# Kernel tuning notes

Hardware: AMD Instinct MI355X
Metric: run time of the kernel (lower is better)

## Reference

```python
import jax, jax.numpy as jnp
import numpy as np
from jax import lax

B, C, H, W = 8, 64, 128, 128
KS = 3          # kernel size
K = KS * KS     # kernel field = 9
PAD = 1


def conv2d(x, w, b):
    # x: [B,Cin,H,W], w: [Cout,Cin,kh,kw], 'same' 3x3 conv
    y = lax.conv_general_dilated(x, w, window_strides=(1, 1),
                                 padding=((PAD, PAD), (PAD, PAD)),
                                 dimension_numbers=('NCHW', 'OIHW', 'NCHW'))
    return y + b[None, :, None, None]


def modulated_deform_conv(x, offset, mask, weight, bias):
    # x:[B,C,H,W], offset:[B,2K,H,W] (dy,dx per tap), mask:[B,K,H,W]
    Bs, Cin, Hin, Win = x.shape
    off = offset.reshape(Bs, K, 2, Hin, Win)
    ky, kx = jnp.meshgrid(jnp.arange(KS), jnp.arange(KS), indexing='ij')
    ky = ky.reshape(K).astype(x.dtype)   # kernel tap row offsets 0..2
    kx = kx.reshape(K).astype(x.dtype)
    # sampling positions p = p0 + p_k + offset (stride=1, pad=1)
    py = (jnp.arange(Hin, dtype=x.dtype)[None, None, :, None] - PAD
          + ky[None, :, None, None] + off[:, :, 0])            # [B,K,H,W]
    px = (jnp.arange(Win, dtype=x.dtype)[None, None, None, :] - PAD
          + kx[None, :, None, None] + off[:, :, 1])            # [B,K,H,W]

    y0 = jnp.floor(py); x0 = jnp.floor(px)
    ly = py - y0; lx = px - x0                                  # frac parts
    y0i = y0.astype(jnp.int32); x0i = x0.astype(jnp.int32)

    x_flat = x.reshape(Bs, Cin, Hin * Win)

    def gather(iy, ix):
        valid = ((iy >= 0) & (iy < Hin) & (ix >= 0) & (ix < Win))
        flat = (jnp.clip(iy, 0, Hin - 1) * Win + jnp.clip(ix, 0, Win - 1))
        g = jax.vmap(lambda xb, ib: xb[:, ib])(x_flat, flat.reshape(Bs, -1))
        g = g.reshape(Bs, Cin, K, Hin, Win)
        return g * valid[:, None].astype(x.dtype)

    w00 = ((1 - ly) * (1 - lx))[:, None]  # [B,1,K,H,W]
    w01 = ((1 - ly) * lx)[:, None]
    w10 = (ly * (1 - lx))[:, None]
    w11 = (ly * lx)[:, None]

    val = (w00 * gather(y0i, x0i) + w01 * gather(y0i, x0i + 1)
           + w10 * gather(y0i + 1, x0i) + w11 * gather(y0i + 1, x0i + 1))
    val = val * mask[:, None]                                   # modulation
    out = jnp.einsum('ock,bckhw->bohw', weight.reshape(weight.shape[0], Cin, K), val)
    return out + bias[None, :, None, None]


def setup_inputs() -> dict:
    key = jax.random.key(0)
    ks = jax.random.split(key, 7)
    s = 0.05
    return {
        'x': jax.random.normal(ks[0], (B, C, H, W), jnp.float32),
        'w_om': jax.random.normal(ks[1], (3 * K, C, KS, KS), jnp.float32) * s,
        'b_om': jax.random.normal(ks[2], (3 * K,), jnp.float32) * s,
        'w_dc': jax.random.normal(ks[3], (C, C, KS, KS), jnp.float32) * s,
        'b_dc': jax.random.normal(ks[4], (C,), jnp.float32) * s,
        'w_c': jax.random.normal(ks[5], (C, C, KS, KS), jnp.float32) * s,
        'b_c': jax.random.normal(ks[6], (C,), jnp.float32) * s,
    }


def reference(x, w_om, b_om, w_dc, b_dc, w_c, b_c):
    om = conv2d(x, w_om, b_om)                       # [B,3K,H,W]
    offset, mask_raw = om[:, :2 * K], om[:, 2 * K:]
    mask = 2.0 * jax.nn.sigmoid(mask_raw)
    out = modulated_deform_conv(x, offset, mask, w_dc, b_dc)
    act = jnp.where(out > 0, out, 0.2 * out)         # LeakyReLU(0.2)
    return conv2d(act, w_c, b_c) + x
```

## Files before the change

### kernel.cpp

```cpp
#include <hip/hip_runtime.h>
#include <math.h>

#define Bn 8
#define Cn 64
#define Hn 128
#define Wn 128
#define HWn (Hn * Wn)

#define WOM_OFF 0
#define WDC_OFF 18432
#define WC_OFF 55296

typedef __attribute__((ext_vector_type(8))) short short8;
typedef __attribute__((ext_vector_type(4))) float floatx4;

__device__ __forceinline__ float bf2f(short s) {
  return __uint_as_float(((unsigned)(unsigned short)s) << 16);
}
__device__ __forceinline__ short f2bf(float f) {
  unsigned u = __float_as_uint(f);
  u += 0x7fff + ((u >> 16) & 1);
  return (short)(u >> 16);
}

__global__ __launch_bounds__(256) void k_prep_w(
    const float* __restrict__ w_om, const float* __restrict__ w_dc,
    const float* __restrict__ w_c, short* __restrict__ wt) {
  int idx = blockIdx.x * 256 + threadIdx.x;
  if (idx >= 92160) return;
  float v;
  if (idx < WDC_OFF) {
    int e = idx;
    int elem = e & 7, lane = (e >> 3) & 63, mt = (e >> 9) & 1, t = e >> 10;
    int kk = t % 9, cc = t / 9;
    int row = mt * 16 + (lane & 15);
    int cin = cc * 32 + (lane >> 4) * 8 + elem;
    v = (row < 27) ? w_om[(row * 64 + cin) * 9 + kk] : 0.f;
  } else {
    int e = (idx < WC_OFF) ? idx - WDC_OFF : idx - WC_OFF;
    const float* src = (idx < WC_OFF) ? w_dc : w_c;
    int elem = e & 7, lane = (e >> 3) & 63, mt = (e >> 9) & 3, t = e >> 11;
    int kk = t % 9, cc = t / 9;
    int row = mt * 16 + (lane & 15);
    int cin = cc * 32 + (lane >> 4) * 8 + elem;
    v = src[(row * 64 + cin) * 9 + kk];
  }
  wt[idx] = f2bf(v);
}

__global__ __launch_bounds__(256) void k_prep_x(const float* __restrict__ x,
                                                short* __restrict__ xT) {
  __shared__ float tile[64][129];
  const int bid = blockIdx.x;
  const int b = bid & 7, h = bid >> 3;
  const int tid = threadIdx.x;
  const float* xb = x + (size_t)b * 64 * HWn + h * Wn;
  for (int i = tid; i < 8192; i += 256) {
    int c = i >> 7, w = i & 127;
    tile[c][w] = xb[c * HWn + w];
  }
  __syncthreads();
  short* dst = xT + ((size_t)(b * Hn + h) * Wn) * 64;
  for (int i = tid; i < 2048; i += 256) {
    int w = i >> 4, c4 = (i & 15) * 4;
    short4 o;
    o.x = f2bf(tile[c4 + 0][w]);
    o.y = f2bf(tile[c4 + 1][w]);
    o.z = f2bf(tile[c4 + 2][w]);
    o.w = f2bf(tile[c4 + 3][w]);
    *(short4*)(dst + (size_t)w * 64 + c4) = o;
  }
}

__global__ __launch_bounds__(256, 3) void k_omdef(
    const short* __restrict__ xT, const short* __restrict__ wt,
    const float* __restrict__ b_om, const float* __restrict__ b_dc,
    short* __restrict__ actT) {
  __shared__ __attribute__((aligned(16))) short lw[18432];
  __shared__ float som[27 * 66];
  __shared__ unsigned sbw[4 * 576];
  unsigned* sb01 = sbw;
  unsigned* sb23 = sbw + 576;
  unsigned* sw01 = sbw + 1152;
  unsigned* sw23 = sbw + 1728;

  const int bid = blockIdx.x;
  const int b = bid & 7;
  const int r = bid >> 3;
  const int h = r >> 1, w0 = (r & 1) * 64;
  const int tid = threadIdx.x;
  const int wave = tid >> 6, lane = tid & 63, quad = lane >> 4, lr = lane & 15;
  const short* xb = xT + (size_t)b * HWn * 64;
  const int pxl = wave * 16 + lr;
  const int gxp = w0 + pxl;

  floatx4 zf = {0.f, 0.f, 0.f, 0.f};

  {
    const short8* src = (const short8*)(wt + WOM_OFF);
    short8* dst = (short8*)lw;
    for (int i = tid; i < 2304; i += 256) dst[i] = src[i];
  }
  __syncthreads();

  floatx4 aco[2] = {zf, zf};
#pragma unroll 3
  for (int kk = 0; kk < 9; ++kk) {
    int ky = kk / 3, kx = kk - ky * 3;
    int gy = h + ky - 1, gx = gxp + kx - 1;
    bool ok = ((unsigned)gy < (unsigned)Hn) && ((unsigned)gx < (unsigned)Wn);
    int gyc = min(max(gy, 0), Hn - 1), gxc = min(max(gx, 0), Wn - 1);
    const short* rec = xb + (size_t)(gyc * Wn + gxc) * 64 + quad * 8;
#pragma unroll
    for (int cc = 0; cc < 2; ++cc) {
      short8 bf = *(const short8*)(rec + cc * 32);
      if (!ok) bf = (short8){0, 0, 0, 0, 0, 0, 0, 0};
      short8 a0 = *(const short8*)&lw[((cc * 9 + kk) * 2 + 0) * 512 + lane * 8];
      short8 a1 = *(const short8*)&lw[((cc * 9 + kk) * 2 + 1) * 512 + lane * 8];
      aco[0] = __builtin_amdgcn_mfma_f32_16x16x32_bf16(a0, bf, aco[0], 0, 0, 0);
      aco[1] = __builtin_amdgcn_mfma_f32_16x16x32_bf16(a1, bf, aco[1], 0, 0, 0);
    }
  }
#pragma unroll
  for (int mt = 0; mt < 2; ++mt) {
#pragma unroll
    for (int rr = 0; rr < 4; ++rr) {
      int co = mt * 16 + quad * 4 + rr;
      if (co < 27) {
        float v = aco[mt][rr] + b_om[co];
        if (co >= 18) v = 2.f / (1.f + expf(-v));
        som[co * 66 + pxl] = v;
      }
    }
  }
  __syncthreads();

  {
    const short8* src = (const short8*)(wt + WDC_OFF);
    short8* dst = (short8*)lw;
    for (int i = tid; i < 2304; i += 256) dst[i] = src[i];
  }
  for (int pr = tid; pr < 576; pr += 256) {
    int k = pr >> 6, p = pr & 63;
    float offy = som[(2 * k) * 66 + p];
    float offx = som[(2 * k + 1) * 66 + p];
    float m = som[(18 + k) * 66 + p];
    float py = (float)(h - 1 + (k / 3)) + offy;
    float px_ = (float)(w0 + p - 1 + (k % 3)) + offx;
    float fy = floorf(py), fx = floorf(px_);
    float ly = py - fy, lx = px_ - fx;
    int iy0 = (int)fy, ix0 = (int)fx;
    int iy1 = iy0 + 1, ix1 = ix0 + 1;
    bool vy0 = (iy0 >= 0) && (iy0 < Hn);
    bool vy1 = (iy1 >= 0) && (iy1 < Hn);
    bool vx0 = (ix0 >= 0) && (ix0 < Wn);
    bool vx1 = (ix1 >= 0) && (ix1 < Wn);
    unsigned cy0 = (unsigned)min(max(iy0, 0), Hn - 1);
    unsigned cy1 = (unsigned)min(max(iy1, 0), Hn - 1);
    unsigned cx0 = (unsigned)min(max(ix0, 0), Wn - 1);
    unsigned cx1 = (unsigned)min(max(ix1, 0), Wn - 1);
    sb01[pr] = (cy0 * Wn + cx0) | ((cy0 * Wn + cx1) << 16);
    sb23[pr] = (cy1 * Wn + cx0) | ((cy1 * Wn + cx1) << 16);
    float u0 = (vy0 && vx0) ? (1.f - ly) * (1.f - lx) * m : 0.f;
    float u1 = (vy0 && vx1) ? (1.f - ly) * lx * m : 0.f;
    float u2 = (vy1 && vx0) ? ly * (1.f - lx) * m : 0.f;
    float u3 = (vy1 && vx1) ? ly * lx * m : 0.f;
    sw01[pr] = (unsigned)(unsigned short)f2bf(u0) |
               ((unsigned)(unsigned short)f2bf(u1) << 16);
    sw23[pr] = (unsigned)(unsigned short)f2bf(u2) |
               ((unsigned)(unsigned short)f2bf(u3) << 16);
  }
  __syncthreads();

  floatx4 acc[4] = {zf, zf, zf, zf};
  for (int cc = 0; cc < 2; ++cc) {
    if (cc) {
      __syncthreads();
      const short8* src = (const short8*)(wt + WDC_OFF + 18432);
      short8* dst = (short8*)lw;
      for (int i = tid; i < 2304; i += 256) dst[i] = src[i];
      __syncthreads();
    }
#pragma unroll 3
    for (int kk = 0; kk < 9; ++kk) {
      int pr = kk * 64 + pxl;
      unsigned a01 = sb01[pr], a23 = sb23[pr];
      unsigned uw01 = sw01[pr], uw23 = sw23[pr];
      float u0 = bf2f((short)(uw01 & 0xFFFF));
      float u1 = bf2f((short)(uw01 >> 16));
      float u2 = bf2f((short)(uw23 & 0xFFFF));
      float u3 = bf2f((short)(uw23 >> 16));
      int co = cc * 32 + quad * 8;
      short8 q0 = *(const short8*)(xb + (size_t)(a01 & 0xFFFF) * 64 + co);
      short8 q1 = *(const short8*)(xb + (size_t)(a01 >> 16) * 64 + co);
      short8 q2 = *(const short8*)(xb + (size_t)(a23 & 0xFFFF) * 64 + co);
      short8 q3 = *(const short8*)(xb + (size_t)(a23 >> 16) * 64 + co);
      short8 bf;
#pragma unroll
      for (int e = 0; e < 8; ++e) {
        float f = u0 * bf2f(q0[e]) + u1 * bf2f(q1[e]) + u2 * bf2f(q2[e]) +
                  u3 * bf2f(q3[e]);
        bf[e] = f2bf(f);
      }
#pragma unroll
      for (int mt = 0; mt < 4; ++mt) {
        short8 am = *(const short8*)&lw[(kk * 4 + mt) * 512 + lane * 8];
        acc[mt] = __builtin_amdgcn_mfma_f32_16x16x32_bf16(am, bf, acc[mt], 0, 0, 0);
      }
    }
  }

  short* ab = actT + ((size_t)(b * Hn + h) * Wn + w0) * 64;
#pragma unroll
  for (int mt = 0; mt < 4; ++mt) {
    int c0 = mt * 16 + quad * 4;
    short4 o;
    float v;
    v = acc[mt][0] + b_dc[c0 + 0]; o.x = f2bf(v > 0.f ? v : 0.2f * v);
    v = acc[mt][1] + b_dc[c0 + 1]; o.y = f2bf(v > 0.f ? v : 0.2f * v);
    v = acc[mt][2] + b_dc[c0 + 2]; o.z = f2bf(v > 0.f ? v : 0.2f * v);
    v = acc[mt][3] + b_dc[c0 + 3]; o.w = f2bf(v > 0.f ? v : 0.2f * v);
    *(short4*)(ab + (size_t)pxl * 64 + c0) = o;
  }
}

__global__ __launch_bounds__(256, 4) void k_conv_out(
    const short* __restrict__ actT, const short* __restrict__ wt,
    const float* __restrict__ b_c, const float* __restrict__ x,
    float* __restrict__ out) {
  __shared__ __attribute__((aligned(16))) short lw[18432];

  const int bid = blockIdx.x;
  const int b = bid & 7;
  const int r = bid >> 3;
  const int h = r >> 1, w0 = (r & 1) * 64;
  const int tid = threadIdx.x;
  const int wave = tid >> 6, lane = tid & 63, quad = lane >> 4, lr = lane & 15;
  const short* ab = actT + (size_t)b * HWn * 64;
  const int pxl = wave * 16 + lr;
  const int gxp = w0 + pxl;

  floatx4 zf = {0.f, 0.f, 0.f, 0.f};
  floatx4 acc[4] = {zf, zf, zf, zf};

  for (int cc = 0; cc < 2; ++cc) {
    if (cc) __syncthreads();
    {
      const short8* src = (const short8*)(wt + WC_OFF + cc * 18432);
      short8* dst = (short8*)lw;
      for (int i = tid; i < 2304; i += 256) dst[i] = src[i];
    }
    __syncthreads();
#pragma unroll 3
    for (int kk = 0; kk < 9; ++kk) {
      int ky = kk / 3, kx = kk - ky * 3;
      int gy = h + ky - 1, gx = gxp + kx - 1;
      bool ok = ((unsigned)gy < (unsigned)Hn) && ((unsigned)gx < (unsigned)Wn);
      int gyc = min(max(gy, 0), Hn - 1), gxc = min(max(gx, 0), Wn - 1);
      short8 bf = *(const short8*)(ab + (size_t)(gyc * Wn + gxc) * 64 +
                                   cc * 32 + quad * 8);
      if (!ok) bf = (short8){0, 0, 0, 0, 0, 0, 0, 0};
#pragma unroll
      for (int mt = 0; mt < 4; ++mt) {
        short8 am = *(const short8*)&lw[(kk * 4 + mt) * 512 + lane * 8];
        acc[mt] = __builtin_amdgcn_mfma_f32_16x16x32_bf16(am, bf, acc[mt], 0, 0, 0);
      }
    }
  }
  __syncthreads();

  float* ot = (float*)lw;
#pragma unroll
  for (int mt = 0; mt < 4; ++mt) {
#pragma unroll
    for (int rr = 0; rr < 4; ++rr) {
      ot[(mt * 16 + quad * 4 + rr) * 66 + pxl] = acc[mt][rr];
    }
  }
  __syncthreads();

  const int row = tid >> 2, seg = tid & 3;
  const float bias = b_c[row];
  const size_t gbase = ((size_t)(b * 64 + row) * Hn + h) * Wn + w0 + seg * 16;
  const float* xr = x + gbase;
  float* op = out + gbase;
#pragma unroll
  for (int j = 0; j < 4; ++j) {
    floatx4 t = *(const floatx4*)&ot[row * 66 + seg * 16 + j * 4];
    floatx4 xv = *(const floatx4*)&xr[j * 4];
    t = t + xv;
    t[0] += bias; t[1] += bias; t[2] += bias; t[3] += bias;
    *(floatx4*)&op[j * 4] = t;
  }
}

extern "C" void kernel_launch(void* const* d_in, const int* in_sizes, int n_in,
                              void* d_out, int out_size, void* d_ws,
                              size_t ws_size, hipStream_t stream) {
  const float* x = (const float*)d_in[0];
  const float* w_om = (const float*)d_in[1];
  const float* b_om = (const float*)d_in[2];
  const float* w_dc = (const float*)d_in[3];
  const float* b_dc = (const float*)d_in[4];
  const float* w_c = (const float*)d_in[5];
  const float* b_c = (const float*)d_in[6];
  float* out = (float*)d_out;

  short* xT = (short*)d_ws;
  short* actT = xT + (size_t)Bn * HWn * 64;
  short* wt = actT + (size_t)Bn * HWn * 64;

  k_prep_w<<<dim3(360), 256, 0, stream>>>(w_om, w_dc, w_c, wt);
  k_prep_x<<<dim3(1024), 256, 0, stream>>>(x, xT);
  k_omdef<<<dim3(2048), 256, 0, stream>>>(xT, wt, b_om, b_dc, actT);
  k_conv_out<<<dim3(2048), 256, 0, stream>>>(actT, wt, b_c, x, out);
}
```

Baseline: 231.1 us.

## Stage weights via async global-to-LDS loads and batch gathers ahead of MFMAs

```diff
diff --git a/kernel.cpp b/kernel.cpp
--- a/kernel.cpp
+++ b/kernel.cpp
@@ -13,6 +13,7 @@
 
 typedef __attribute__((ext_vector_type(8))) short short8;
 typedef __attribute__((ext_vector_type(4))) float floatx4;
+typedef __attribute__((ext_vector_type(2))) float float2v;
 
 __device__ __forceinline__ float bf2f(short s) {
   return __uint_as_float(((unsigned)(unsigned short)s) << 16);
@@ -21,6 +22,16 @@
   unsigned u = __float_as_uint(f);
   u += 0x7fff + ((u >> 16) & 1);
   return (short)(u >> 16);
+}
+
+__device__ __forceinline__ void gl_lds16(const short* g, short* l) {
+  __builtin_amdgcn_global_load_lds(
+      (const __attribute__((address_space(1))) unsigned int*)(const void*)g,
+      (__attribute__((address_space(3))) unsigned int*)(void*)l, 16, 0, 0);
+}
+__device__ __forceinline__ void stage_async(const short* src, short* dst,
+                                            int n16, int tid) {
+  for (int i = tid; i < n16; i += 256) gl_lds16(src + i * 8, dst + i * 8);
 }
 
 __global__ __launch_bounds__(256) void k_prep_w(
@@ -78,11 +89,6 @@
     short* __restrict__ actT) {
   __shared__ __attribute__((aligned(16))) short lw[18432];
   __shared__ float som[27 * 66];
-  __shared__ unsigned sbw[4 * 576];
-  unsigned* sb01 = sbw;
-  unsigned* sb23 = sbw + 576;
-  unsigned* sw01 = sbw + 1152;
-  unsigned* sw23 = sbw + 1728;
 
   const int bid = blockIdx.x;
   const int b = bid & 7;
@@ -93,32 +99,35 @@
   const short* xb = xT + (size_t)b * HWn * 64;
   const int pxl = wave * 16 + lr;
   const int gxp = w0 + pxl;
-
-  floatx4 zf = {0.f, 0.f, 0.f, 0.f};
-
-  {
-    const short8* src = (const short8*)(wt + WOM_OFF);
-    short8* dst = (short8*)lw;
-    for (int i = tid; i < 2304; i += 256) dst[i] = src[i];
-  }
-  __syncthreads();
-
-  floatx4 aco[2] = {zf, zf};
-#pragma unroll 3
+  const floatx4 zf = {0.f, 0.f, 0.f, 0.f};
+  const short8 z8 = {0, 0, 0, 0, 0, 0, 0, 0};
+
+  stage_async(wt + WOM_OFF, lw, 2304, tid);
+
+  short8 Bom[18];
+#pragma unroll
   for (int kk = 0; kk < 9; ++kk) {
     int ky = kk / 3, kx = kk - ky * 3;
     int gy = h + ky - 1, gx = gxp + kx - 1;
     bool ok = ((unsigned)gy < (unsigned)Hn) && ((unsigned)gx < (unsigned)Wn);
     int gyc = min(max(gy, 0), Hn - 1), gxc = min(max(gx, 0), Wn - 1);
     const short* rec = xb + (size_t)(gyc * Wn + gxc) * 64 + quad * 8;
+    short8 v0 = *(const short8*)rec;
+    short8 v1 = *(const short8*)(rec + 32);
+    Bom[kk * 2 + 0] = ok ? v0 : z8;
+    Bom[kk * 2 + 1] = ok ? v1 : z8;
+  }
+  __syncthreads();
+
+  floatx4 aco[2] = {zf, zf};
+#pragma unroll
+  for (int kk = 0; kk < 9; ++kk) {
 #pragma unroll
     for (int cc = 0; cc < 2; ++cc) {
-      short8 bf = *(const short8*)(rec + cc * 32);
-      if (!ok) bf = (short8){0, 0, 0, 0, 0, 0, 0, 0};
       short8 a0 = *(const short8*)&lw[((cc * 9 + kk) * 2 + 0) * 512 + lane * 8];
       short8 a1 = *(const short8*)&lw[((cc * 9 + kk) * 2 + 1) * 512 + lane * 8];
-      aco[0] = __builtin_amdgcn_mfma_f32_16x16x32_bf16(a0, bf, aco[0], 0, 0, 0);
-      aco[1] = __builtin_amdgcn_mfma_f32_16x16x32_bf16(a1, bf, aco[1], 0, 0, 0);
+      aco[0] = __builtin_amdgcn_mfma_f32_16x16x32_bf16(a0, Bom[kk * 2 + cc], aco[0], 0, 0, 0);
+      aco[1] = __builtin_amdgcn_mfma_f32_16x16x32_bf16(a1, Bom[kk * 2 + cc], aco[1], 0, 0, 0);
     }
   }
 #pragma unroll
@@ -135,18 +144,16 @@
   }
   __syncthreads();
 
-  {
-    const short8* src = (const short8*)(wt + WDC_OFF);
-    short8* dst = (short8*)lw;
-    for (int i = tid; i < 2304; i += 256) dst[i] = src[i];
-  }
-  for (int pr = tid; pr < 576; pr += 256) {
-    int k = pr >> 6, p = pr & 63;
-    float offy = som[(2 * k) * 66 + p];
-    float offx = som[(2 * k + 1) * 66 + p];
-    float m = som[(18 + k) * 66 + p];
+  stage_async(wt + WDC_OFF, lw, 2304, tid);
+
+  unsigned qa01[9], qa23[9], qw01[9], qw23[9];
+#pragma unroll
+  for (int k = 0; k < 9; ++k) {
+    float offy = som[(2 * k) * 66 + pxl];
+    float offx = som[(2 * k + 1) * 66 + pxl];
+    float m = som[(18 + k) * 66 + pxl];
     float py = (float)(h - 1 + (k / 3)) + offy;
-    float px_ = (float)(w0 + p - 1 + (k % 3)) + offx;
+    float px_ = (float)(gxp - 1 + (k % 3)) + offx;
     float fy = floorf(py), fx = floorf(px_);
     float ly = py - fy, lx = px_ - fx;
     int iy0 = (int)fy, ix0 = (int)fx;
@@ -159,16 +166,16 @@
     unsigned cy1 = (unsigned)min(max(iy1, 0), Hn - 1);
     unsigned cx0 = (unsigned)min(max(ix0, 0), Wn - 1);
     unsigned cx1 = (unsigned)min(max(ix1, 0), Wn - 1);
-    sb01[pr] = (cy0 * Wn + cx0) | ((cy0 * Wn + cx1) << 16);
-    sb23[pr] = (cy1 * Wn + cx0) | ((cy1 * Wn + cx1) << 16);
+    qa01[k] = (cy0 * Wn + cx0) | ((cy0 * Wn + cx1) << 16);
+    qa23[k] = (cy1 * Wn + cx0) | ((cy1 * Wn + cx1) << 16);
     float u0 = (vy0 && vx0) ? (1.f - ly) * (1.f - lx) * m : 0.f;
     float u1 = (vy0 && vx1) ? (1.f - ly) * lx * m : 0.f;
     float u2 = (vy1 && vx0) ? ly * (1.f - lx) * m : 0.f;
     float u3 = (vy1 && vx1) ? ly * lx * m : 0.f;
-    sw01[pr] = (unsigned)(unsigned short)f2bf(u0) |
-               ((unsigned)(unsigned short)f2bf(u1) << 16);
-    sw23[pr] = (unsigned)(unsigned short)f2bf(u2) |
-               ((unsigned)(unsigned short)f2bf(u3) << 16);
+    qw01[k] = (unsigned)(unsigned short)f2bf(u0) |
+              ((unsigned)(unsigned short)f2bf(u1) << 16);
+    qw23[k] = (unsigned)(unsigned short)f2bf(u2) |
+              ((unsigned)(unsigned short)f2bf(u3) << 16);
   }
   __syncthreads();
 
@@ -176,36 +183,47 @@
   for (int cc = 0; cc < 2; ++cc) {
     if (cc) {
       __syncthreads();
-      const short8* src = (const short8*)(wt + WDC_OFF + 18432);
-      short8* dst = (short8*)lw;
-      for (int i = tid; i < 2304; i += 256) dst[i] = src[i];
-      __syncthreads();
-    }
-#pragma unroll 3
-    for (int kk = 0; kk < 9; ++kk) {
-      int pr = kk * 64 + pxl;
-      unsigned a01 = sb01[pr], a23 = sb23[pr];
-      unsigned uw01 = sw01[pr], uw23 = sw23[pr];
-      float u0 = bf2f((short)(uw01 & 0xFFFF));
-      float u1 = bf2f((short)(uw01 >> 16));
-      float u2 = bf2f((short)(uw23 & 0xFFFF));
-      float u3 = bf2f((short)(uw23 >> 16));
-      int co = cc * 32 + quad * 8;
-      short8 q0 = *(const short8*)(xb + (size_t)(a01 & 0xFFFF) * 64 + co);
-      short8 q1 = *(const short8*)(xb + (size_t)(a01 >> 16) * 64 + co);
-      short8 q2 = *(const short8*)(xb + (size_t)(a23 & 0xFFFF) * 64 + co);
-      short8 q3 = *(const short8*)(xb + (size_t)(a23 >> 16) * 64 + co);
-      short8 bf;
-#pragma unroll
-      for (int e = 0; e < 8; ++e) {
-        float f = u0 * bf2f(q0[e]) + u1 * bf2f(q1[e]) + u2 * bf2f(q2[e]) +
-                  u3 * bf2f(q3[e]);
-        bf[e] = f2bf(f);
+      stage_async(wt + WDC_OFF + 18432, lw, 2304, tid);
+    }
+    const short* xbc = xb + cc * 32 + quad * 8;
+    short8 Bset[9];
+#pragma unroll
+    for (int k = 0; k < 9; ++k) {
+      unsigned a01 = qa01[k], a23 = qa23[k];
+      short8 q0 = *(const short8*)(xbc + (size_t)(a01 & 0xFFFFu) * 64);
+      short8 q1 = *(const short8*)(xbc + (size_t)(a01 >> 16) * 64);
+      short8 q2 = *(const short8*)(xbc + (size_t)(a23 & 0xFFFFu) * 64);
+      short8 q3 = *(const short8*)(xbc + (size_t)(a23 >> 16) * 64);
+      float2v u0 = {__uint_as_float(qw01[k] << 16), __uint_as_float(qw01[k] << 16)};
+      float2v u1 = {__uint_as_float(qw01[k] & 0xFFFF0000u), __uint_as_float(qw01[k] & 0xFFFF0000u)};
+      float2v u2 = {__uint_as_float(qw23[k] << 16), __uint_as_float(qw23[k] << 16)};
+      float2v u3 = {__uint_as_float(qw23[k] & 0xFFFF0000u), __uint_as_float(qw23[k] & 0xFFFF0000u)};
+      const unsigned* d0 = (const unsigned*)&q0;
+      const unsigned* d1 = (const unsigned*)&q1;
+      const unsigned* d2 = (const unsigned*)&q2;
+      const unsigned* d3 = (const unsigned*)&q3;
+      short8 o;
+      unsigned* od = (unsigned*)&o;
+#pragma unroll
+      for (int j = 0; j < 4; ++j) {
+        float2v f0 = {__uint_as_float(d0[j] << 16), __uint_as_float(d0[j] & 0xFFFF0000u)};
+        float2v f1 = {__uint_as_float(d1[j] << 16), __uint_as_float(d1[j] & 0xFFFF0000u)};
+        float2v f2 = {__uint_as_float(d2[j] << 16), __uint_as_float(d2[j] & 0xFFFF0000u)};
+        float2v f3 = {__uint_as_float(d3[j] << 16), __uint_as_float(d3[j] & 0xFFFF0000u)};
+        float2v s = f0 * u0 + f1 * u1 + f2 * u2 + f3 * u3;
+        unsigned lo = __float_as_uint(s.x) + 0x8000u;
+        unsigned hi = __float_as_uint(s.y) + 0x8000u;
+        od[j] = __builtin_amdgcn_perm(hi, lo, 0x07060302);
       }
+      Bset[k] = o;
+    }
+    if (cc) __syncthreads();
+#pragma unroll
+    for (int k = 0; k < 9; ++k) {
 #pragma unroll
       for (int mt = 0; mt < 4; ++mt) {
-        short8 am = *(const short8*)&lw[(kk * 4 + mt) * 512 + lane * 8];
-        acc[mt] = __builtin_amdgcn_mfma_f32_16x16x32_bf16(am, bf, acc[mt], 0, 0, 0);
+        short8 a = *(const short8*)&lw[(k * 4 + mt) * 512 + lane * 8];
+        acc[mt] = __builtin_amdgcn_mfma_f32_16x16x32_bf16(a, Bset[k], acc[mt], 0, 0, 0);
       }
     }
   }
@@ -239,36 +257,46 @@
   const short* ab = actT + (size_t)b * HWn * 64;
   const int pxl = wave * 16 + lr;
   const int gxp = w0 + pxl;
-
-  floatx4 zf = {0.f, 0.f, 0.f, 0.f};
+  const floatx4 zf = {0.f, 0.f, 0.f, 0.f};
+  const short8 z8 = {0, 0, 0, 0, 0, 0, 0, 0};
+
+  stage_async(wt + WC_OFF, lw, 2304, tid);
+
   floatx4 acc[4] = {zf, zf, zf, zf};
-
   for (int cc = 0; cc < 2; ++cc) {
-    if (cc) __syncthreads();
-    {
-      const short8* src = (const short8*)(wt + WC_OFF + cc * 18432);
-      short8* dst = (short8*)lw;
-      for (int i = tid; i < 2304; i += 256) dst[i] = src[i];
-    }
-    __syncthreads();
-#pragma unroll 3
+    if (cc) {
+      __syncthreads();
+      stage_async(wt + WC_OFF + 18432, lw, 2304, tid);
+    }
+    const short* abc = ab + cc * 32 + quad * 8;
+    short8 Bc[9];
+#pragma unroll
     for (int kk = 0; kk < 9; ++kk) {
       int ky = kk / 3, kx = kk - ky * 3;
       int gy = h + ky - 1, gx = gxp + kx - 1;
       bool ok = ((unsigned)gy < (unsigned)Hn) && ((unsigned)gx < (unsigned)Wn);
       int gyc = min(max(gy, 0), Hn - 1), gxc = min(max(gx, 0), Wn - 1);
-      short8 bf = *(const short8*)(ab + (size_t)(gyc * Wn + gxc) * 64 +
-                                   cc * 32 + quad * 8);
-      if (!ok) bf = (short8){0, 0, 0, 0, 0, 0, 0, 0};
+      short8 v = *(const short8*)(abc + (size_t)(gyc * Wn + gxc) * 64);
+      Bc[kk] = ok ? v : z8;
+    }
+    __syncthreads();
+#pragma unroll
+    for (int kk = 0; kk < 9; ++kk) {
 #pragma unroll
       for (int mt = 0; mt < 4; ++mt) {
-        short8 am = *(const short8*)&lw[(kk * 4 + mt) * 512 + lane * 8];
-        acc[mt] = __builtin_amdgcn_mfma_f32_16x16x32_bf16(am, bf, acc[mt], 0, 0, 0);
+        short8 a = *(const short8*)&lw[(kk * 4 + mt) * 512 + lane * 8];
+        acc[mt] = __builtin_amdgcn_mfma_f32_16x16x32_bf16(a, Bc[kk], acc[mt], 0, 0, 0);
       }
     }
   }
-  __syncthreads();
-
+
+  const int row = tid >> 2, seg = tid & 3;
+  const size_t gbase = ((size_t)(b * 64 + row) * Hn + h) * Wn + w0 + seg * 16;
+  floatx4 xr[4];
+#pragma unroll
+  for (int j = 0; j < 4; ++j) xr[j] = *(const floatx4*)(x + gbase + j * 4);
+
+  __syncthreads();
   float* ot = (float*)lw;
 #pragma unroll
   for (int mt = 0; mt < 4; ++mt) {
@@ -279,16 +307,12 @@
   }
   __syncthreads();
 
-  const int row = tid >> 2, seg = tid & 3;
   const float bias = b_c[row];
-  const size_t gbase = ((size_t)(b * 64 + row) * Hn + h) * Wn + w0 + seg * 16;
-  const float* xr = x + gbase;
   float* op = out + gbase;
 #pragma unroll
   for (int j = 0; j < 4; ++j) {
     floatx4 t = *(const floatx4*)&ot[row * 66 + seg * 16 + j * 4];
-    floatx4 xv = *(const floatx4*)&xr[j * 4];
-    t = t + xv;
+    t = t + xr[j];
     t[0] += bias; t[1] += bias; t[2] += bias; t[3] += bias;
     *(floatx4*)&op[j * 4] = t;
   }
```

After: 348.0 us. 50.6% more time.
